# Performance work log

Measured on AMD Instinct MI355X. Metric: run time of the kernel, lower is better.

Reference implementation:

```python
import jax, jax.numpy as jnp
import numpy as np

C = 768
E = 32
H = 4 * C

def setup_inputs() -> dict:
    key = jax.random.key(0)
    ks = jax.random.split(key, 5)
    B, T = 2, 1024
    scale_in = 1.0 / np.sqrt(C)
    scale_hid = 1.0 / np.sqrt(H)
    return {
        "x": jax.random.normal(ks[0], (B, T, C), jnp.float32),
        "gate_w": jax.random.normal(ks[1], (C, E), jnp.float32) * scale_in,
        "gate_b": jnp.zeros((E,), jnp.float32),
        "w1": jax.random.normal(ks[2], (E, C, H), jnp.float32) * scale_in,
        "b1": jnp.zeros((E, H), jnp.float32),
        "w2": jax.random.normal(ks[3], (E, H, C), jnp.float32) * scale_hid,
        "b2": jnp.zeros((E, C), jnp.float32),
    }

def reference(x, gate_w, gate_b, w1, b1, w2, b2):
    # gates: [B, T, E] softmax over experts
    gates = jax.nn.softmax(x @ gate_w + gate_b, axis=-1)
    # all-expert FFN: h [B, T, E, H]
    h = jax.nn.gelu(jnp.einsum('btc,ech->bteh', x, w1) + b1, approximate=False)
    # expert outputs [B, T, E, C]
    y = jnp.einsum('bteh,ehc->btec', h, w2) + b2
    # gate-weighted sum over experts -> [B, T, C]  (dropout = identity in eval)
    out = jnp.einsum('bte,btec->btc', gates, y)
    return out
```

## Files before the change

kernel.cpp:

```cpp
#include <hip/hip_runtime.h>
#include <stdint.h>


typedef unsigned short u16;
typedef __attribute__((ext_vector_type(8))) short short8;
typedef __attribute__((ext_vector_type(8))) unsigned short ushort8v;
typedef __attribute__((ext_vector_type(4))) unsigned short ushort4v;
typedef __attribute__((ext_vector_type(4))) float float4v;

#define DEV __device__ __forceinline__

DEV u16 rne_bf16(float f) {
  union { float f; uint32_t u; } v; v.f = f;
  uint32_t u = v.u;
  u += 0x7FFFu + ((u >> 16) & 1u);
  return (u16)(u >> 16);
}

DEV float fast_erf(float x) {
  float ax = __builtin_fabsf(x);
  float t = __builtin_amdgcn_rcpf(__builtin_fmaf(0.3275911f, ax, 1.0f));
  float p = t * (0.254829592f + t * (-0.284496736f + t * (1.421413741f +
            t * (-1.453152027f + t * 1.061405429f))));
  float r = 1.0f - p * __expf(-ax * ax);
  return __builtin_copysignf(r, x);
}

DEV void load_lds16(const void* g, void* l) {
  __builtin_amdgcn_global_load_lds(
      (const __attribute__((address_space(1))) unsigned int*)g,
      (__attribute__((address_space(3))) unsigned int*)l,
      16, 0, 0);
}


__global__ void cvt_x_kernel(const float* __restrict__ x, u16* __restrict__ xb, int n4) {
  int i = blockIdx.x * 256 + threadIdx.x;
  if (i >= n4) return;
  float4v v = *(const float4v*)(x + (size_t)i * 4);
  ushort4v o;
  o[0] = rne_bf16(v[0]); o[1] = rne_bf16(v[1]);
  o[2] = rne_bf16(v[2]); o[3] = rne_bf16(v[3]);
  *(ushort4v*)(xb + (size_t)i * 4) = o;
}

__global__ void gate_kernel(const float* __restrict__ x, const float* __restrict__ gw,
                            const float* __restrict__ gb, float* __restrict__ gates) {
  int lane = threadIdx.x;
  int tok = blockIdx.x * 2 + (lane >> 5);
  int e = lane & 31;
  const float* xr = x + (size_t)tok * 768;
  float s = gb[e];
  #pragma unroll 4
  for (int c = 0; c < 768; ++c) s += xr[c] * gw[c * 32 + e];
  float mx = s;
  #pragma unroll
  for (int o = 16; o >= 1; o >>= 1) mx = fmaxf(mx, __shfl_xor(mx, o, 32));
  float ex = __expf(s - mx);
  float sum = ex;
  #pragma unroll
  for (int o = 16; o >= 1; o >>= 1) sum += __shfl_xor(sum, o, 32);
  gates[tok * 32 + e] = ex / sum;
}

__global__ void bias_out_kernel(const float* __restrict__ gates, const float* __restrict__ b2,
                                float* __restrict__ out) {
  int idx = blockIdx.x * 256 + threadIdx.x;
  int n = idx / 768;
  int c = idx - n * 768;
  const float* g = gates + n * 32;
  float s = 0.f;
  #pragma unroll
  for (int e = 0; e < 32; ++e) s += g[e] * b2[e * 768 + c];
  out[idx] = s;
}

__global__ void reduce_kernel(const float* __restrict__ part, float* __restrict__ out, int n4) {
  int i = blockIdx.x * 256 + threadIdx.x;
  if (i >= n4) return;
  float4v o = *(const float4v*)(out + (size_t)i * 4);
  #pragma unroll
  for (int z = 0; z < 8; ++z) {
    float4v p = *(const float4v*)(part + (size_t)z * (2048L * 768) + (size_t)i * 4);
    o[0] += p[0]; o[1] += p[1]; o[2] += p[2]; o[3] += p[3];
  }
  *(float4v*)(out + (size_t)i * 4) = o;
}

__global__ void pack_b_kernel(const float* __restrict__ in, u16* __restrict__ out,
                              int ktiles, int n_per_e, long e_stride, int row_stride) {
  int kt = blockIdx.x, nt = blockIdx.y;
  int n0 = nt * 128;
  int e = n0 / n_per_e;
  int nl = n0 - e * n_per_e;
  const float* src = in + (long)e * e_stride + (long)kt * 64 * row_stride + nl;

  __shared__ u16 lds[64 * 136];
  int t = threadIdx.x;
  {
    int k = t >> 2, nq = (t & 3) * 32;
    const float* p = src + (long)k * row_stride + nq;
    u16 tmp[32];
    #pragma unroll
    for (int i = 0; i < 32; i += 4) {
      float4v v = *(const float4v*)(p + i);
      tmp[i] = rne_bf16(v[0]); tmp[i + 1] = rne_bf16(v[1]);
      tmp[i + 2] = rne_bf16(v[2]); tmp[i + 3] = rne_bf16(v[3]);
    }
    #pragma unroll
    for (int i = 0; i < 32; i += 8)
      *(ushort8v*)&lds[k * 136 + nq + i] = *(ushort8v*)&tmp[i];
  }
  __syncthreads();
  {
    int n = t >> 1, half = t & 1;
    u16 v[32];
    #pragma unroll
    for (int j = 0; j < 32; ++j) v[j] = lds[(half * 32 + j) * 136 + n];
    u16* tile = out + ((long)nt * ktiles + kt) * 8192 + n * 64;
    int sw = n & 7;
    #pragma unroll
    for (int cc = 0; cc < 4; ++cc) {
      int c = half * 4 + cc;
      *(ushort8v*)(tile + ((c ^ sw) * 8)) = *(ushort8v*)&v[cc * 8];
    }
  }
}

template <int MODE>
__global__ __launch_bounds__(256) void gemm_tile(
    const u16* __restrict__ A, long lda,
    const u16* __restrict__ Bp, int ktiles_total, int nkt,
    void* __restrict__ outp, long ldo,
    const float* __restrict__ gates, const float* __restrict__ b1, int e_base) {

  __shared__ u16 As[128 * 64];
  __shared__ u16 Bs[128 * 64];
  __shared__ float gbuf[128];

  const int tid = threadIdx.x;
  const int wave = tid >> 6;
  const int lane = tid & 63;
  const int wr = wave >> 1, wc = wave & 1;
  const int m0 = blockIdx.x * 128;
  const int n0 = blockIdx.y * 128;
  const int kt_begin = blockIdx.z * nkt;

  float4v acc[4][4] = {};

  const int lr = lane >> 3, l8 = lane & 7;
  const u16* gA = A + (long)(m0 + wave * 32 + lr) * lda + (long)kt_begin * 64
                    + (long)(l8 ^ lr) * 8;
  const u16* gB = Bp + ((long)blockIdx.y * ktiles_total + kt_begin) * 8192
                     + wave * 2048 + lane * 8;
  u16* ldsA0 = &As[wave * 2048];
  u16* ldsB0 = &Bs[wave * 2048];

  const int frow = lane & 15;
  const int fq = lane >> 4;
  const int fxor = lane & 7;

  for (int kt = 0; kt < nkt; ++kt) {
    __syncthreads();
    #pragma unroll
    for (int j = 0; j < 4; ++j) {
      load_lds16(gA + (long)j * 8 * lda, ldsA0 + j * 512);
      load_lds16(gB + j * 512,           ldsB0 + j * 512);
    }
    gA += 64; gB += 8192;
    __syncthreads();

    #pragma unroll
    for (int s = 0; s < 2; ++s) {
      const int co = ((s * 4 + fq) ^ fxor) * 8;
      short8 af[4], bf[4];
      #pragma unroll
      for (int i = 0; i < 4; ++i)
        af[i] = *(const short8*)&As[(wr * 64 + i * 16 + frow) * 64 + co];
      #pragma unroll
      for (int i = 0; i < 4; ++i)
        bf[i] = *(const short8*)&Bs[(wc * 64 + i * 16 + frow) * 64 + co];
      #pragma unroll
      for (int mi = 0; mi < 4; ++mi)
        #pragma unroll
        for (int ni = 0; ni < 4; ++ni)
          acc[mi][ni] = __builtin_amdgcn_mfma_f32_16x16x32_bf16(af[mi], bf[ni], acc[mi][ni], 0, 0, 0);
    }
  }

  if (MODE == 1) {
    int e_loc = n0 / 3072;
    int h0 = n0 - e_loc * 3072;
    int eg = e_base + e_loc;
    if (tid < 128) gbuf[tid] = gates[(m0 + tid) * 32 + eg];
    __syncthreads();
    u16* out = (u16*)outp;
    const float* b1e = b1 + (long)eg * 3072 + h0;
    #pragma unroll
    for (int ni = 0; ni < 4; ++ni) {
      int ncol = wc * 64 + ni * 16 + frow;
      float bv = b1e[ncol];
      #pragma unroll
      for (int mi = 0; mi < 4; ++mi) {
        #pragma unroll
        for (int r = 0; r < 4; ++r) {
          int mrow = wr * 64 + mi * 16 + fq * 4 + r;
          float v = acc[mi][ni][r] + bv;
          v = 0.5f * v * (1.0f + fast_erf(v * 0.70710678118654752440f));
          v *= gbuf[mrow];
          out[(long)(m0 + mrow) * ldo + (n0 + ncol)] = rne_bf16(v);
        }
      }
    }
  } else {
    float* out = (float*)outp + (long)blockIdx.z * (2048L * 768);
    #pragma unroll
    for (int ni = 0; ni < 4; ++ni) {
      int ncol = n0 + wc * 64 + ni * 16 + frow;
      #pragma unroll
      for (int mi = 0; mi < 4; ++mi) {
        #pragma unroll
        for (int r = 0; r < 4; ++r) {
          int mrow = m0 + wr * 64 + mi * 16 + fq * 4 + r;
          out[(long)mrow * ldo + ncol] = acc[mi][ni][r];
        }
      }
    }
  }
}


extern "C" void kernel_launch(void* const* d_in, const int* in_sizes, int n_in,
                              void* d_out, int out_size, void* d_ws, size_t ws_size,
                              hipStream_t stream) {
  (void)in_sizes; (void)n_in; (void)out_size;
  const float* x  = (const float*)d_in[0];
  const float* gw = (const float*)d_in[1];
  const float* gb = (const float*)d_in[2];
  const float* w1 = (const float*)d_in[3];
  const float* b1 = (const float*)d_in[4];
  const float* w2 = (const float*)d_in[5];
  const float* b2 = (const float*)d_in[6];
  float* out = (float*)d_out;

  const long N = 2048, C = 768, H = 3072;

  const long base_need = N * C * 2 + N * 32 * 4 + 8L * N * C * 4;
  int G = 32;
  while (G > 1 && (size_t)(base_need + (long)G * (C * H * 2 * 2 + N * H * 2)) > ws_size) G >>= 1;

  char* p = (char*)d_ws;
  u16*   xb    = (u16*)p;   p += N * C * 2;
  float* gates = (float*)p; p += N * 32 * 4;
  float* parts = (float*)p; p += 8L * N * C * 4;
  u16*   w1b   = (u16*)p;   p += (long)G * C * H * 2;
  u16*   w2b   = (u16*)p;   p += (long)G * H * C * 2;
  u16*   hbuf  = (u16*)p;

  cvt_x_kernel<<<(N * C / 4 + 255) / 256, 256, 0, stream>>>(x, xb, (int)(N * C / 4));
  gate_kernel<<<N / 2, 64, 0, stream>>>(x, gw, gb, gates);
  bias_out_kernel<<<N * C / 256, 256, 0, stream>>>(gates, b2, out);

  const int ngroups = 32 / G;
  for (int g = 0; g < ngroups; ++g) {
    const float* w1g = w1 + (long)g * G * C * H;
    const float* w2g = w2 + (long)g * G * H * C;

    dim3 pg1(12, 24 * G);
    pack_b_kernel<<<pg1, 256, 0, stream>>>(w1g, w1b, 12, (int)H, (long)C * H, (int)H);

    dim3 gg1(16, 24 * G, 1);
    gemm_tile<1><<<gg1, 256, 0, stream>>>(xb, C, w1b, 12, 12,
                                          (void*)hbuf, (long)G * H, gates, b1, g * G);

    dim3 pg2(48 * G, 6);
    pack_b_kernel<<<pg2, 256, 0, stream>>>(w2g, w2b, 48 * G, 768, 0L, 768);

    dim3 gg2(16, 6, 8);
    gemm_tile<2><<<gg2, 256, 0, stream>>>(hbuf, (long)G * H, w2b, 48 * G, 6 * G,
                                          (void*)parts, 768, nullptr, nullptr, 0);

    reduce_kernel<<<(int)((N * C / 4 + 255) / 256), 256, 0, stream>>>(parts, out, (int)(N * C / 4));
  }
}
```

Measured before the change: 1.702 ms.

## Use 256x256 double-buffered GEMM tiles and move gating into per-expert reduction

Replaces the 128x128 single-buffered GEMM with a 512-thread 256x256 tile kernel. It double-buffers LDS through 128KB of dynamic shared memory and interleaves quarter-tile MFMA blocks with barriers and priority hints so global loads overlap compute. The second GEMM now splits K per expert (grid z = G), so the gate weighting moves out of the first GEMM epilogue into the reduction, which multiplies each expert partial by its gate. This raises partial-buffer workspace to G×N×C floats and reduction traffic from 8 to G slices, and it needs enough LDS for two blocks per CU.

New measurement: 1.669 ms. No clear change (-2.0%).

```diff
diff --git a/kernel.cpp b/kernel.cpp
--- a/kernel.cpp
+++ b/kernel.cpp
@@ -75,14 +75,18 @@
   out[idx] = s;
 }
 
-__global__ void reduce_kernel(const float* __restrict__ part, float* __restrict__ out, int n4) {
+__global__ void reduce_kernel(const float* __restrict__ part, const float* __restrict__ gates,
+                              float* __restrict__ out, int zn, int e_base, int n4) {
   int i = blockIdx.x * 256 + threadIdx.x;
   if (i >= n4) return;
+  int n = (i << 2) / 768;
+  const float* g = gates + n * 32 + e_base;
   float4v o = *(const float4v*)(out + (size_t)i * 4);
-  #pragma unroll
-  for (int z = 0; z < 8; ++z) {
+  #pragma unroll 4
+  for (int z = 0; z < zn; ++z) {
+    float gz = g[z];
     float4v p = *(const float4v*)(part + (size_t)z * (2048L * 768) + (size_t)i * 4);
-    o[0] += p[0]; o[1] += p[1]; o[2] += p[2]; o[3] += p[3];
+    o[0] += gz * p[0]; o[1] += gz * p[1]; o[2] += gz * p[2]; o[3] += gz * p[3];
   }
   *(float4v*)(out + (size_t)i * 4) = o;
 }
@@ -128,104 +132,138 @@
 }
 
 template <int MODE>
-__global__ __launch_bounds__(256) void gemm_tile(
+__global__ __launch_bounds__(512, 2) void gemm256(
     const u16* __restrict__ A, long lda,
-    const u16* __restrict__ Bp, int ktiles_total, int nkt,
+    const u16* __restrict__ Bp, int ktt, int ktb, int nkt,
     void* __restrict__ outp, long ldo,
-    const float* __restrict__ gates, const float* __restrict__ b1, int e_base) {
-
-  __shared__ u16 As[128 * 64];
-  __shared__ u16 Bs[128 * 64];
-  __shared__ float gbuf[128];
-
-  const int tid = threadIdx.x;
-  const int wave = tid >> 6;
-  const int lane = tid & 63;
-  const int wr = wave >> 1, wc = wave & 1;
-  const int m0 = blockIdx.x * 128;
-  const int n0 = blockIdx.y * 128;
-  const int kt_begin = blockIdx.z * nkt;
-
-  float4v acc[4][4] = {};
-
+    const float* __restrict__ b1g, long zstride) {
+
+  extern __shared__ u16 sm[];
+  u16* const Abuf[2] = { sm,         sm + 32768 };
+  u16* const Bbuf[2] = { sm + 16384, sm + 49152 };
+
+  const int tid  = threadIdx.x;
+  const int wave = tid >> 6, lane = tid & 63;
+  const int wr = wave >> 2, wc = wave & 3;
+  const int bh = wave >> 2, w4 = wave & 3;
   const int lr = lane >> 3, l8 = lane & 7;
-  const u16* gA = A + (long)(m0 + wave * 32 + lr) * lda + (long)kt_begin * 64
-                    + (long)(l8 ^ lr) * 8;
-  const u16* gB = Bp + ((long)blockIdx.y * ktiles_total + kt_begin) * 8192
-                     + wave * 2048 + lane * 8;
-  u16* ldsA0 = &As[wave * 2048];
-  u16* ldsB0 = &Bs[wave * 2048];
-
-  const int frow = lane & 15;
-  const int fq = lane >> 4;
-  const int fxor = lane & 7;
-
-  for (int kt = 0; kt < nkt; ++kt) {
-    __syncthreads();
-    #pragma unroll
-    for (int j = 0; j < 4; ++j) {
-      load_lds16(gA + (long)j * 8 * lda, ldsA0 + j * 512);
-      load_lds16(gB + j * 512,           ldsB0 + j * 512);
-    }
-    gA += 64; gB += 8192;
-    __syncthreads();
-
-    #pragma unroll
-    for (int s = 0; s < 2; ++s) {
-      const int co = ((s * 4 + fq) ^ fxor) * 8;
-      short8 af[4], bf[4];
+  const int frow = lane & 15, fq = lane >> 4, fx = lane & 7;
+  const int m0 = blockIdx.x * 256;
+  const int nt0 = blockIdx.y * 2;
+  const int kt_begin = blockIdx.z * ktb;
+
+  const u16* gA = A + (long)(m0 + wave * 32 + lr) * lda + (long)kt_begin * 64 + (l8 ^ lr) * 8;
+  const u16* gB = Bp + ((long)(nt0 + bh) * ktt + kt_begin) * 8192 + w4 * 2048 + lane * 8;
+  u16* const ldsA[2] = { Abuf[0] + wave * 2048, Abuf[1] + wave * 2048 };
+  u16* const ldsB[2] = { Bbuf[0] + bh * 8192 + w4 * 2048, Bbuf[1] + bh * 8192 + w4 * 2048 };
+
+  float4v acc[8][4] = {};
+  short8 af[4][2], bf[2][2];
+
+#define STAGE(p) { \
+    _Pragma("unroll") for (int j = 0; j < 4; ++j) { \
+      load_lds16(gA + (long)j * 8 * lda, ldsA[p] + j * 512); \
+      load_lds16(gB + j * 512,           ldsB[p] + j * 512); } \
+    gA += 64; gB += 8192; }
+
+#define RD_A(p, QM) \
+    _Pragma("unroll") for (int mf = 0; mf < 4; ++mf) \
+    _Pragma("unroll") for (int ks = 0; ks < 2; ++ks) \
+      af[mf][ks] = *(const short8*)&Abuf[p][(wr * 128 + (QM) * 64 + mf * 16 + frow) * 64 + \
+                                            (((ks * 4 + fq) ^ fx) * 8)];
+
+#define RD_B(p, QN) \
+    _Pragma("unroll") for (int nf = 0; nf < 2; ++nf) \
+    _Pragma("unroll") for (int ks = 0; ks < 2; ++ks) \
+      bf[nf][ks] = *(const short8*)&Bbuf[p][(wc * 64 + (QN) * 32 + nf * 16 + frow) * 64 + \
+                                            (((ks * 4 + fq) ^ fx) * 8)];
+
+#define MMQ(QM, QN) { \
+    __builtin_amdgcn_s_barrier(); \
+    asm volatile("s_waitcnt lgkmcnt(0)" ::: "memory"); \
+    __builtin_amdgcn_sched_barrier(0); \
+    __builtin_amdgcn_s_setprio(1); \
+    _Pragma("unroll") for (int mf = 0; mf < 4; ++mf) \
+    _Pragma("unroll") for (int nf = 0; nf < 2; ++nf) \
+    _Pragma("unroll") for (int ks = 0; ks < 2; ++ks) \
+      acc[(QM) * 4 + mf][(QN) * 2 + nf] = __builtin_amdgcn_mfma_f32_16x16x32_bf16( \
+          af[mf][ks], bf[nf][ks], acc[(QM) * 4 + mf][(QN) * 2 + nf], 0, 0, 0); \
+    __builtin_amdgcn_s_setprio(0); \
+    __builtin_amdgcn_s_barrier(); }
+
+#define HALF(p) { RD_A(p, 0); RD_B(p, 0); MMQ(0, 0); \
+                  RD_B(p, 1);             MMQ(0, 1); \
+                  RD_A(p, 1);             MMQ(1, 1); \
+                  RD_B(p, 0);             MMQ(1, 0); }
+
+#define WAITV8 { asm volatile("s_waitcnt vmcnt(8)" ::: "memory"); \
+                 __builtin_amdgcn_s_barrier(); __builtin_amdgcn_sched_barrier(0); }
+#define WAITV0 { asm volatile("s_waitcnt vmcnt(0)" ::: "memory"); \
+                 __builtin_amdgcn_s_barrier(); __builtin_amdgcn_sched_barrier(0); }
+
+  STAGE(0); STAGE(1);
+  const int niter = nkt >> 1;
+  for (int i = 0; i < niter - 1; ++i) {
+    WAITV8;
+    HALF(0);
+    STAGE(0);
+    WAITV8;
+    HALF(1);
+    STAGE(1);
+  }
+  WAITV8; HALF(0);
+  WAITV0; HALF(1);
+
+#undef STAGE
+#undef RD_A
+#undef RD_B
+#undef MMQ
+#undef HALF
+#undef WAITV8
+#undef WAITV0
+
+  if (MODE == 1) {
+    const int n0 = nt0 * 128;
+    const int e_loc = n0 / 3072;
+    const int h0 = n0 - e_loc * 3072;
+    const float* be = b1g + (long)e_loc * 3072 + h0;
+    u16* out = (u16*)outp;
+    #pragma unroll
+    for (int qn = 0; qn < 2; ++qn)
       #pragma unroll
-      for (int i = 0; i < 4; ++i)
-        af[i] = *(const short8*)&As[(wr * 64 + i * 16 + frow) * 64 + co];
+      for (int nf = 0; nf < 2; ++nf) {
+        const int ncol = wc * 64 + qn * 32 + nf * 16 + frow;
+        const float bv = be[ncol];
+        #pragma unroll
+        for (int qm = 0; qm < 2; ++qm)
+          #pragma unroll
+          for (int mf = 0; mf < 4; ++mf) {
+            u16* op = out + (long)(m0 + wr * 128 + qm * 64 + mf * 16 + fq * 4) * ldo + (n0 + ncol);
+            #pragma unroll
+            for (int r = 0; r < 4; ++r) {
+              float v = acc[qm * 4 + mf][qn * 2 + nf][r] + bv;
+              v = 0.5f * v * (1.0f + fast_erf(v * 0.70710678118654752440f));
+              op[(long)r * ldo] = rne_bf16(v);
+            }
+          }
+      }
+  } else {
+    float* out = (float*)outp + (long)blockIdx.z * zstride;
+    const int n0 = nt0 * 128;
+    #pragma unroll
+    for (int qn = 0; qn < 2; ++qn)
       #pragma unroll
-      for (int i = 0; i < 4; ++i)
-        bf[i] = *(const short8*)&Bs[(wc * 64 + i * 16 + frow) * 64 + co];
-      #pragma unroll
-      for (int mi = 0; mi < 4; ++mi)
+      for (int nf = 0; nf < 2; ++nf) {
+        const int ncol = n0 + wc * 64 + qn * 32 + nf * 16 + frow;
         #pragma unroll
-        for (int ni = 0; ni < 4; ++ni)
-          acc[mi][ni] = __builtin_amdgcn_mfma_f32_16x16x32_bf16(af[mi], bf[ni], acc[mi][ni], 0, 0, 0);
-    }
-  }
-
-  if (MODE == 1) {
-    int e_loc = n0 / 3072;
-    int h0 = n0 - e_loc * 3072;
-    int eg = e_base + e_loc;
-    if (tid < 128) gbuf[tid] = gates[(m0 + tid) * 32 + eg];
-    __syncthreads();
-    u16* out = (u16*)outp;
-    const float* b1e = b1 + (long)eg * 3072 + h0;
-    #pragma unroll
-    for (int ni = 0; ni < 4; ++ni) {
-      int ncol = wc * 64 + ni * 16 + frow;
-      float bv = b1e[ncol];
-      #pragma unroll
-      for (int mi = 0; mi < 4; ++mi) {
-        #pragma unroll
-        for (int r = 0; r < 4; ++r) {
-          int mrow = wr * 64 + mi * 16 + fq * 4 + r;
-          float v = acc[mi][ni][r] + bv;
-          v = 0.5f * v * (1.0f + fast_erf(v * 0.70710678118654752440f));
-          v *= gbuf[mrow];
-          out[(long)(m0 + mrow) * ldo + (n0 + ncol)] = rne_bf16(v);
-        }
+        for (int qm = 0; qm < 2; ++qm)
+          #pragma unroll
+          for (int mf = 0; mf < 4; ++mf) {
+            float* op = out + (long)(m0 + wr * 128 + qm * 64 + mf * 16 + fq * 4) * ldo + ncol;
+            #pragma unroll
+            for (int r = 0; r < 4; ++r) op[(long)r * ldo] = acc[qm * 4 + mf][qn * 2 + nf][r];
+          }
       }
-    }
-  } else {
-    float* out = (float*)outp + (long)blockIdx.z * (2048L * 768);
-    #pragma unroll
-    for (int ni = 0; ni < 4; ++ni) {
-      int ncol = n0 + wc * 64 + ni * 16 + frow;
-      #pragma unroll
-      for (int mi = 0; mi < 4; ++mi) {
-        #pragma unroll
-        for (int r = 0; r < 4; ++r) {
-          int mrow = m0 + wr * 64 + mi * 16 + fq * 4 + r;
-          out[(long)mrow * ldo + ncol] = acc[mi][ni][r];
-        }
-      }
-    }
   }
 }
 
@@ -245,17 +283,26 @@
 
   const long N = 2048, C = 768, H = 3072;
 
-  const long base_need = N * C * 2 + N * 32 * 4 + 8L * N * C * 4;
   int G = 32;
-  while (G > 1 && (size_t)(base_need + (long)G * (C * H * 2 * 2 + N * H * 2)) > ws_size) G >>= 1;
+  for (;;) {
+    long need = N * C * 2 + N * 32 * 4 + (long)G * N * C * 4
+              + (long)G * C * H * 2 * 2 + N * (long)G * H * 2;
+    if ((size_t)need <= ws_size || G == 1) break;
+    G >>= 1;
+  }
 
   char* p = (char*)d_ws;
   u16*   xb    = (u16*)p;   p += N * C * 2;
   float* gates = (float*)p; p += N * 32 * 4;
-  float* parts = (float*)p; p += 8L * N * C * 4;
+  float* parts = (float*)p; p += (long)G * N * C * 4;
   u16*   w1b   = (u16*)p;   p += (long)G * C * H * 2;
   u16*   w2b   = (u16*)p;   p += (long)G * H * C * 2;
   u16*   hbuf  = (u16*)p;
+
+  hipFuncSetAttribute(reinterpret_cast<const void*>(gemm256<1>),
+                      hipFuncAttributeMaxDynamicSharedMemorySize, 131072);
+  hipFuncSetAttribute(reinterpret_cast<const void*>(gemm256<2>),
+                      hipFuncAttributeMaxDynamicSharedMemorySize, 131072);
 
   cvt_x_kernel<<<(N * C / 4 + 255) / 256, 256, 0, stream>>>(x, xb, (int)(N * C / 4));
   gate_kernel<<<N / 2, 64, 0, stream>>>(x, gw, gb, gates);
@@ -269,17 +316,16 @@
     dim3 pg1(12, 24 * G);
     pack_b_kernel<<<pg1, 256, 0, stream>>>(w1g, w1b, 12, (int)H, (long)C * H, (int)H);
 
-    dim3 gg1(16, 24 * G, 1);
-    gemm_tile<1><<<gg1, 256, 0, stream>>>(xb, C, w1b, 12, 12,
-                                          (void*)hbuf, (long)G * H, gates, b1, g * G);
+    gemm256<1><<<dim3(8, 12 * G, 1), 512, 131072, stream>>>(
+        xb, C, w1b, 12, 0, 12, (void*)hbuf, (long)G * H, b1 + (long)g * G * H, 0L);
 
     dim3 pg2(48 * G, 6);
     pack_b_kernel<<<pg2, 256, 0, stream>>>(w2g, w2b, 48 * G, 768, 0L, 768);
 
-    dim3 gg2(16, 6, 8);
-    gemm_tile<2><<<gg2, 256, 0, stream>>>(hbuf, (long)G * H, w2b, 48 * G, 6 * G,
-                                          (void*)parts, 768, nullptr, nullptr, 0);
-
-    reduce_kernel<<<(int)((N * C / 4 + 255) / 256), 256, 0, stream>>>(parts, out, (int)(N * C / 4));
-  }
-}
+    gemm256<2><<<dim3(8, 3, G), 512, 131072, stream>>>(
+        hbuf, (long)G * H, w2b, 48 * G, 48, 48, (void*)parts, 768L, nullptr, N * C);
+
+    reduce_kernel<<<(int)((N * C / 4 + 255) / 256), 256, 0, stream>>>(
+        parts, gates, out, G, g * G, (int)(N * C / 4));
+  }
+}
```
